# Kernel optimization log

Measured on AMD Instinct MI355X. Metric: run time of the kernel, lower is better.

## Reference

```python
import jax, jax.numpy as jnp
import numpy as np

T = 30
NUM_CLASSES = 2
N = 1048576
EPS = 1e-15


def setup_inputs() -> dict:
    key = jax.random.key(0)
    k1, k2, k3, k4 = jax.random.split(key, 4)
    logit = jax.random.normal(k1, (N, NUM_CLASSES), dtype=jnp.float32)
    # variance must be positive (sqrt/exp); uniform in [0.01, 1)
    var = jax.random.uniform(k2, (N, 1), dtype=jnp.float32, minval=0.01, maxval=1.0)
    true = jax.random.randint(k3, (N,), 0, NUM_CLASSES)
    # standard-normal noise for the T Monte Carlo samples (reparameterized)
    noise = jax.random.normal(k4, (T, N, NUM_CLASSES), dtype=jnp.float32)
    return {"logit": logit, "var": var, "true": true, "noise": noise}


def _mean_ce(logits, labels):
    # CrossEntropyLoss with mean reduction over the batch dim(s)
    lp = jax.nn.log_softmax(logits, axis=-1)
    picked = jnp.take_along_axis(lp, labels[..., None], axis=-1)  # [..., N, 1]
    return -jnp.mean(picked)


def reference(logit, var, true, noise):
    std = jnp.sqrt(var) + EPS                  # [N, 1]
    variance_depressor = jnp.exp(var) - 1.0    # [N, 1]
    undistorted_loss = _mean_ce(logit + EPS, true)  # scalar

    # torch Normal.sample() is non-differentiable -> stop_gradient on std
    eps = jax.lax.stop_gradient(std)[None, :, :] * noise  # [T, N, 2]
    distorted = logit[None, :, :] + EPS + eps              # [T, N, 2]
    lp = jax.nn.log_softmax(distorted, axis=-1)            # [T, N, 2]
    lbl = jnp.broadcast_to(true[None, :, None], (T, true.shape[0], 1))
    distorted_loss = -jnp.mean(jnp.take_along_axis(lp, lbl, axis=-1), axis=(1, 2))  # [T]

    monte_carlo = -jax.nn.elu(undistorted_loss - distorted_loss)  # [T]
    variance_loss = jnp.mean(monte_carlo) * undistorted_loss      # scalar
    loss_final = variance_loss + undistorted_loss + variance_depressor  # [N, 1]
    return jnp.mean(loss_final)
```

## Files before the change

kernel.cpp:

```cpp
#include <hip/hip_runtime.h>
#include <math.h>

#define TSAMP 30
#define FEPS 1e-15f

__device__ __forceinline__ float softplus(float x) {
    float m = fmaxf(x, 0.0f);
    return m + __logf(__expf(x - m) + __expf(-m));
}

__global__ __launch_bounds__(256) void bcc_partial(
    const float4* __restrict__ logit4,
    const float2* __restrict__ var2,
    const int2*   __restrict__ true2,
    const float4* __restrict__ noise4,
    float* __restrict__ partial,
    int npair, int nblk)
{
    float acc[TSAMP];
    #pragma unroll
    for (int t = 0; t < TSAMP; ++t) acc[t] = 0.0f;
    float u_acc = 0.0f, vd_acc = 0.0f;

    const int stride = gridDim.x * blockDim.x;
    for (int p = blockIdx.x * blockDim.x + threadIdx.x; p < npair; p += stride) {
        const float4 lg = logit4[p];
        const float2 v  = var2[p];
        const int2   yy = true2[p];

        const float sg0 = yy.x ? 1.0f : -1.0f;
        const float d0  = sg0 * (lg.x - lg.y);
        const float ss0 = sg0 * (__fsqrt_rn(v.x) + FEPS);
        const float sg1 = yy.y ? 1.0f : -1.0f;
        const float d1  = sg1 * (lg.z - lg.w);
        const float ss1 = sg1 * (__fsqrt_rn(v.y) + FEPS);

        vd_acc += (__expf(v.x) - 1.0f) + (__expf(v.y) - 1.0f);
        u_acc  -= softplus(d0) + softplus(d1);

        const float4* nptr = noise4 + p;
        #pragma unroll
        for (int t = 0; t < TSAMP; ++t) {
            const float4 nz = nptr[(size_t)t * (size_t)npair];
            const float x0 = fmaf(ss0, nz.x - nz.y, d0);
            const float x1 = fmaf(ss1, nz.z - nz.w, d1);
            acc[t] -= softplus(x0) + softplus(x1);
        }
    }

    __shared__ float s_part[4][32];
    const int lane = threadIdx.x & 63;
    const int wav  = threadIdx.x >> 6;
    #pragma unroll
    for (int a = 0; a < 32; ++a) {
        float vv = (a < TSAMP) ? acc[a] : ((a == TSAMP) ? u_acc : vd_acc);
        #pragma unroll
        for (int off = 32; off >= 1; off >>= 1)
            vv += __shfl_down(vv, off, 64);
        if (lane == 0) s_part[wav][a] = vv;
    }
    __syncthreads();
    if (threadIdx.x < 32) {
        const int a = threadIdx.x;
        const float s = s_part[0][a] + s_part[1][a] + s_part[2][a] + s_part[3][a];
        partial[(size_t)a * (size_t)nblk + blockIdx.x] = s;
    }
}

__global__ __launch_bounds__(256) void bcc_reduce(
    const float* __restrict__ partial,
    int nblk, float* __restrict__ res32)
{
    const int a = blockIdx.x;
    float s = 0.0f;
    for (int j = threadIdx.x; j < nblk; j += 256)
        s += partial[(size_t)a * (size_t)nblk + j];
    #pragma unroll
    for (int off = 32; off >= 1; off >>= 1)
        s += __shfl_down(s, off, 64);
    __shared__ float sw[4];
    if ((threadIdx.x & 63) == 0) sw[threadIdx.x >> 6] = s;
    __syncthreads();
    if (threadIdx.x == 0)
        res32[a] = sw[0] + sw[1] + sw[2] + sw[3];
}

__global__ __launch_bounds__(64) void bcc_epilogue(
    const float* __restrict__ res32, float invN, float* __restrict__ out)
{
    if (threadIdx.x == 0) {
        const float U  = -res32[30] * invN;
        const float vd =  res32[31] * invN;
        float mc_sum = 0.0f;
        #pragma unroll
        for (int t = 0; t < TSAMP; ++t) {
            const float D = -res32[t] * invN;
            const float x = U - D;
            const float e = (x > 0.0f) ? x : expm1f(x);
            mc_sum += -e;
        }
        const float variance_loss = (mc_sum / (float)TSAMP) * U;
        out[0] = variance_loss + U + vd;
    }
}

extern "C" void kernel_launch(void* const* d_in, const int* in_sizes, int n_in,
                              void* d_out, int out_size, void* d_ws, size_t ws_size,
                              hipStream_t stream) {
    const float* logit = (const float*)d_in[0];
    const float* var   = (const float*)d_in[1];
    const int*   tru   = (const int*)d_in[2];
    const float* noise = (const float*)d_in[3];
    float* out = (float*)d_out;

    const int N = in_sizes[1];
    const int npair = N / 2;

    int nblk = 2048;
    const size_t need = (size_t)32 * (size_t)nblk * sizeof(float) + 32 * sizeof(float);
    if (ws_size < need) {
        nblk = (int)((ws_size - 32 * sizeof(float)) / (32 * sizeof(float)));
        if (nblk < 1) nblk = 1;
    }
    float* partial = (float*)d_ws;
    float* res32   = partial + (size_t)32 * (size_t)nblk;

    bcc_partial<<<nblk, 256, 0, stream>>>(
        (const float4*)logit, (const float2*)var, (const int2*)tru,
        (const float4*)noise, partial, npair, nblk);

    bcc_reduce<<<32, 256, 0, stream>>>(partial, nblk, res32);

    bcc_epilogue<<<1, 64, 0, stream>>>(res32, 1.0f / (float)N, out);
}
```

Baseline: 68.38 us.

## Split Monte Carlo samples across block groups and simplify softplus

```diff
diff --git a/kernel.cpp b/kernel.cpp
--- a/kernel.cpp
+++ b/kernel.cpp
@@ -2,11 +2,12 @@
 #include <math.h>
 
 #define TSAMP 30
-#define FEPS 1e-15f
+#define NGRP  5
+#define TPG   6
+#define FEPS  1e-15f
 
 __device__ __forceinline__ float softplus(float x) {
-    float m = fmaxf(x, 0.0f);
-    return m + __logf(__expf(x - m) + __expf(-m));
+    return fmaxf(x, 0.0f) + __logf(1.0f + __expf(-fabsf(x)));
 }
 
 __global__ __launch_bounds__(256) void bcc_partial(
@@ -15,15 +16,21 @@
     const int2*   __restrict__ true2,
     const float4* __restrict__ noise4,
     float* __restrict__ partial,
-    int npair, int nblk)
+    int npair, int pblk)
 {
-    float acc[TSAMP];
+    const int g     = blockIdx.x % NGRP;
+    const int pb    = blockIdx.x / NGRP;
+    const int tbase = g * TPG;
+
+    float acc[TPG];
     #pragma unroll
-    for (int t = 0; t < TSAMP; ++t) acc[t] = 0.0f;
+    for (int k = 0; k < TPG; ++k) acc[k] = 0.0f;
     float u_acc = 0.0f, vd_acc = 0.0f;
 
-    const int stride = gridDim.x * blockDim.x;
-    for (int p = blockIdx.x * blockDim.x + threadIdx.x; p < npair; p += stride) {
+    const int pstride = pblk * 256;
+    const float4* nbase = noise4 + (size_t)tbase * (size_t)npair;
+
+    for (int p = pb * 256 + threadIdx.x; p < npair; p += pstride) {
         const float4 lg = logit4[p];
         const float2 v  = var2[p];
         const int2   yy = true2[p];
@@ -35,46 +42,51 @@
         const float d1  = sg1 * (lg.z - lg.w);
         const float ss1 = sg1 * (__fsqrt_rn(v.y) + FEPS);
 
-        vd_acc += (__expf(v.x) - 1.0f) + (__expf(v.y) - 1.0f);
-        u_acc  -= softplus(d0) + softplus(d1);
+        if (g == 0) {
+            vd_acc += (__expf(v.x) - 1.0f) + (__expf(v.y) - 1.0f);
+            u_acc  -= softplus(d0) + softplus(d1);
+        }
 
-        const float4* nptr = noise4 + p;
+        const float4* nptr = nbase + p;
         #pragma unroll
-        for (int t = 0; t < TSAMP; ++t) {
-            const float4 nz = nptr[(size_t)t * (size_t)npair];
+        for (int k = 0; k < TPG; ++k) {
+            const float4 nz = nptr[(size_t)k * (size_t)npair];
             const float x0 = fmaf(ss0, nz.x - nz.y, d0);
             const float x1 = fmaf(ss1, nz.z - nz.w, d1);
-            acc[t] -= softplus(x0) + softplus(x1);
+            acc[k] -= softplus(x0) + softplus(x1);
         }
     }
 
-    __shared__ float s_part[4][32];
+    __shared__ float s_part[4][TPG + 2];
     const int lane = threadIdx.x & 63;
     const int wav  = threadIdx.x >> 6;
     #pragma unroll
-    for (int a = 0; a < 32; ++a) {
-        float vv = (a < TSAMP) ? acc[a] : ((a == TSAMP) ? u_acc : vd_acc);
+    for (int a = 0; a < TPG + 2; ++a) {
+        float vv = (a < TPG) ? acc[a] : ((a == TPG) ? u_acc : vd_acc);
         #pragma unroll
         for (int off = 32; off >= 1; off >>= 1)
             vv += __shfl_down(vv, off, 64);
         if (lane == 0) s_part[wav][a] = vv;
     }
     __syncthreads();
-    if (threadIdx.x < 32) {
+    if (threadIdx.x < TPG + 2) {
         const int a = threadIdx.x;
         const float s = s_part[0][a] + s_part[1][a] + s_part[2][a] + s_part[3][a];
-        partial[(size_t)a * (size_t)nblk + blockIdx.x] = s;
+        if (a < TPG)
+            partial[(size_t)(tbase + a) * (size_t)pblk + pb] = s;
+        else if (g == 0)
+            partial[(size_t)(TSAMP + (a - TPG)) * (size_t)pblk + pb] = s;
     }
 }
 
 __global__ __launch_bounds__(256) void bcc_reduce(
     const float* __restrict__ partial,
-    int nblk, float* __restrict__ res32)
+    int pblk, float* __restrict__ res32)
 {
     const int a = blockIdx.x;
     float s = 0.0f;
-    for (int j = threadIdx.x; j < nblk; j += 256)
-        s += partial[(size_t)a * (size_t)nblk + j];
+    for (int j = threadIdx.x; j < pblk; j += 256)
+        s += partial[(size_t)a * (size_t)pblk + j];
     #pragma unroll
     for (int off = 32; off >= 1; off >>= 1)
         s += __shfl_down(s, off, 64);
@@ -116,20 +128,24 @@
     const int N = in_sizes[1];
     const int npair = N / 2;
 
-    int nblk = 2048;
-    const size_t need = (size_t)32 * (size_t)nblk * sizeof(float) + 32 * sizeof(float);
-    if (ws_size < need) {
-        nblk = (int)((ws_size - 32 * sizeof(float)) / (32 * sizeof(float)));
-        if (nblk < 1) nblk = 1;
+    int pblk = 1024;
+    {
+        int maxp = (npair + 255) / 256;
+        if (pblk > maxp) pblk = maxp;
+        const size_t need = (size_t)32 * (size_t)pblk * sizeof(float) + 32 * sizeof(float);
+        if (ws_size < need) {
+            pblk = (int)((ws_size - 32 * sizeof(float)) / (32 * sizeof(float)));
+            if (pblk < 1) pblk = 1;
+        }
     }
     float* partial = (float*)d_ws;
-    float* res32   = partial + (size_t)32 * (size_t)nblk;
+    float* res32   = partial + (size_t)32 * (size_t)pblk;
 
-    bcc_partial<<<nblk, 256, 0, stream>>>(
+    bcc_partial<<<NGRP * pblk, 256, 0, stream>>>(
         (const float4*)logit, (const float2*)var, (const int2*)tru,
-        (const float4*)noise, partial, npair, nblk);
+        (const float4*)noise, partial, npair, pblk);
 
-    bcc_reduce<<<32, 256, 0, stream>>>(partial, nblk, res32);
+    bcc_reduce<<<32, 256, 0, stream>>>(partial, pblk, res32);
 
     bcc_epilogue<<<1, 64, 0, stream>>>(res32, 1.0f / (float)N, out);
 }
```

After: 65.58 us. 4.1% less time.

## Parallelize partial kernel over Monte Carlo samples with XCD-aware block mapping

Applied to the files above, without the earlier changes.

```diff
diff --git a/kernel.cpp b/kernel.cpp
--- a/kernel.cpp
+++ b/kernel.cpp
@@ -2,11 +2,12 @@
 #include <math.h>
 
 #define TSAMP 30
-#define FEPS 1e-15f
+#define RPB   1024
+#define ITERS (RPB / 256)
+#define FEPS  1e-15f
 
 __device__ __forceinline__ float softplus(float x) {
-    float m = fmaxf(x, 0.0f);
-    return m + __logf(__expf(x - m) + __expf(-m));
+    return fmaxf(x, 0.0f) + __logf(1.0f + __expf(-fabsf(x)));
 }
 
 __global__ __launch_bounds__(256) void bcc_partial(
@@ -15,66 +16,83 @@
     const int2*   __restrict__ true2,
     const float4* __restrict__ noise4,
     float* __restrict__ partial,
-    int npair, int nblk)
+    int npair, int npr)
 {
-    float acc[TSAMP];
+    int t, pr;
+    if ((npr & 7) == 0) {
+        const int x    = blockIdx.x & 7;
+        const int slot = blockIdx.x >> 3;
+        t  = slot % TSAMP;
+        pr = x * (npr >> 3) + slot / TSAMP;
+    } else {
+        t  = blockIdx.x % TSAMP;
+        pr = blockIdx.x / TSAMP;
+    }
+
+    const float4* nrow = noise4 + (size_t)t * (size_t)npair;
+    const int base = pr * RPB;
+
+    float acc = 0.0f, u_acc = 0.0f, vd_acc = 0.0f;
+
     #pragma unroll
-    for (int t = 0; t < TSAMP; ++t) acc[t] = 0.0f;
-    float u_acc = 0.0f, vd_acc = 0.0f;
+    for (int it = 0; it < ITERS; ++it) {
+        const int p = base + it * 256 + (int)threadIdx.x;
+        if (p < npair) {
+            const float4 nz = nrow[p];
+            const float4 lg = logit4[p];
+            const float2 v  = var2[p];
+            const int2   yy = true2[p];
 
-    const int stride = gridDim.x * blockDim.x;
-    for (int p = blockIdx.x * blockDim.x + threadIdx.x; p < npair; p += stride) {
-        const float4 lg = logit4[p];
-        const float2 v  = var2[p];
-        const int2   yy = true2[p];
+            const float sg0 = yy.x ? 1.0f : -1.0f;
+            const float d0  = sg0 * (lg.x - lg.y);
+            const float ss0 = sg0 * (__fsqrt_rn(v.x) + FEPS);
+            const float sg1 = yy.y ? 1.0f : -1.0f;
+            const float d1  = sg1 * (lg.z - lg.w);
+            const float ss1 = sg1 * (__fsqrt_rn(v.y) + FEPS);
 
-        const float sg0 = yy.x ? 1.0f : -1.0f;
-        const float d0  = sg0 * (lg.x - lg.y);
-        const float ss0 = sg0 * (__fsqrt_rn(v.x) + FEPS);
-        const float sg1 = yy.y ? 1.0f : -1.0f;
-        const float d1  = sg1 * (lg.z - lg.w);
-        const float ss1 = sg1 * (__fsqrt_rn(v.y) + FEPS);
+            acc -= softplus(fmaf(ss0, nz.x - nz.y, d0))
+                 + softplus(fmaf(ss1, nz.z - nz.w, d1));
 
-        vd_acc += (__expf(v.x) - 1.0f) + (__expf(v.y) - 1.0f);
-        u_acc  -= softplus(d0) + softplus(d1);
-
-        const float4* nptr = noise4 + p;
-        #pragma unroll
-        for (int t = 0; t < TSAMP; ++t) {
-            const float4 nz = nptr[(size_t)t * (size_t)npair];
-            const float x0 = fmaf(ss0, nz.x - nz.y, d0);
-            const float x1 = fmaf(ss1, nz.z - nz.w, d1);
-            acc[t] -= softplus(x0) + softplus(x1);
+            if (t == 0) {
+                vd_acc += (__expf(v.x) - 1.0f) + (__expf(v.y) - 1.0f);
+                u_acc  -= softplus(d0) + softplus(d1);
+            }
         }
     }
 
-    __shared__ float s_part[4][32];
+    __shared__ float s_part[4][3];
     const int lane = threadIdx.x & 63;
     const int wav  = threadIdx.x >> 6;
     #pragma unroll
-    for (int a = 0; a < 32; ++a) {
-        float vv = (a < TSAMP) ? acc[a] : ((a == TSAMP) ? u_acc : vd_acc);
+    for (int a = 0; a < 3; ++a) {
+        float vv = (a == 0) ? acc : ((a == 1) ? u_acc : vd_acc);
         #pragma unroll
         for (int off = 32; off >= 1; off >>= 1)
             vv += __shfl_down(vv, off, 64);
         if (lane == 0) s_part[wav][a] = vv;
     }
     __syncthreads();
-    if (threadIdx.x < 32) {
-        const int a = threadIdx.x;
-        const float s = s_part[0][a] + s_part[1][a] + s_part[2][a] + s_part[3][a];
-        partial[(size_t)a * (size_t)nblk + blockIdx.x] = s;
+    if (threadIdx.x == 0) {
+        const float s0 = s_part[0][0] + s_part[1][0] + s_part[2][0] + s_part[3][0];
+        partial[(size_t)t * (size_t)npr + pr] = s0;
+        if (t == 0) {
+            const float s1 = s_part[0][1] + s_part[1][1] + s_part[2][1] + s_part[3][1];
+            const float s2 = s_part[0][2] + s_part[1][2] + s_part[2][2] + s_part[3][2];
+            partial[(size_t)30 * (size_t)npr + pr] = s1;
+            partial[(size_t)31 * (size_t)npr + pr] = s2;
+        }
     }
 }
 
 __global__ __launch_bounds__(256) void bcc_reduce(
     const float* __restrict__ partial,
-    int nblk, float* __restrict__ res32)
+    int npr, float* __restrict__ res32)
 {
     const int a = blockIdx.x;
+    const float* row = partial + (size_t)a * (size_t)npr;
     float s = 0.0f;
-    for (int j = threadIdx.x; j < nblk; j += 256)
-        s += partial[(size_t)a * (size_t)nblk + j];
+    for (int j = threadIdx.x; j < npr; j += 256)
+        s += row[j];
     #pragma unroll
     for (int off = 32; off >= 1; off >>= 1)
         s += __shfl_down(s, off, 64);
@@ -116,20 +134,22 @@
     const int N = in_sizes[1];
     const int npair = N / 2;
 
-    int nblk = 2048;
-    const size_t need = (size_t)32 * (size_t)nblk * sizeof(float) + 32 * sizeof(float);
-    if (ws_size < need) {
-        nblk = (int)((ws_size - 32 * sizeof(float)) / (32 * sizeof(float)));
-        if (nblk < 1) nblk = 1;
+    int npr = (npair + RPB - 1) / RPB;
+    {
+        const size_t need = (size_t)32 * (size_t)npr * sizeof(float) + 32 * sizeof(float);
+        if (ws_size < need) {
+            npr = (int)((ws_size - 32 * sizeof(float)) / (32 * sizeof(float)));
+            if (npr < 1) npr = 1;
+        }
     }
     float* partial = (float*)d_ws;
-    float* res32   = partial + (size_t)32 * (size_t)nblk;
+    float* res32   = partial + (size_t)32 * (size_t)npr;
 
-    bcc_partial<<<nblk, 256, 0, stream>>>(
+    bcc_partial<<<TSAMP * npr, 256, 0, stream>>>(
         (const float4*)logit, (const float2*)var, (const int2*)tru,
-        (const float4*)noise, partial, npair, nblk);
+        (const float4*)noise, partial, npair, npr);
 
-    bcc_reduce<<<32, 256, 0, stream>>>(partial, nblk, res32);
+    bcc_reduce<<<32, 256, 0, stream>>>(partial, npr, res32);
 
     bcc_epilogue<<<1, 64, 0, stream>>>(res32, 1.0f / (float)N, out);
 }
```

Result: faster. 54.80 us, median of 2 (-19.9%).
